# Optimization experiments

Hardware: AMD Instinct MI355X
Metric: run time of the kernel (lower is better)

## Reference

```python
import jax, jax.numpy as jnp
import numpy as np

N = 50000
E = 800000
D = 64


def _gcn_layer(x, row, col, norm, W, b, n_nodes):
    # h = X W  (PyG GCNConv applies linear before propagation, bias after)
    h = x @ W                                   # [N, D]
    msg = norm[:, None] * h[row]                # gather source feats, [E+N, D]
    out = jax.ops.segment_sum(msg, col, num_segments=n_nodes)  # scatter to targets
    return out + b


def _gcn_norm(edge_index, n_nodes, dtype):
    # add self loops with weight 1, symmetric normalization D^-1/2 (A+I) D^-1/2
    sl = jnp.arange(n_nodes, dtype=edge_index.dtype)
    row = jnp.concatenate([edge_index[0], sl])  # source
    col = jnp.concatenate([edge_index[1], sl])  # target
    w = jnp.ones(row.shape[0], dtype=dtype)
    deg = jax.ops.segment_sum(w, col, num_segments=n_nodes)
    dinv = jnp.where(deg > 0, jax.lax.rsqrt(deg), 0.0)
    norm = dinv[row] * dinv[col]                # [E+N]
    return row, col, norm


def setup_inputs() -> dict:
    key = jax.random.key(0)
    k1, k2, k3, k4 = jax.random.split(key, 4)
    x = jax.random.normal(k1, (N, D), dtype=jnp.float32)
    edge_index = jax.random.randint(k2, (2, E), 0, N, dtype=jnp.int64)
    # Glorot-style init like PyG GCNConv lin weights; bias zeros
    s = 1.0 / np.sqrt(D)
    W1 = jax.random.uniform(k3, (D, D), jnp.float32, -s, s)
    W2 = jax.random.uniform(k4, (D, D), jnp.float32, -s, s)
    b1 = jnp.zeros((D,), jnp.float32)
    b2 = jnp.zeros((D,), jnp.float32)
    return {"x": x, "W1": W1, "b1": b1, "W2": W2, "b2": b2, "edge_index": edge_index}


def reference(x, W1, b1, W2, b2, edge_index):
    n_nodes = x.shape[0]
    row, col, norm = _gcn_norm(edge_index, n_nodes, x.dtype)
    z = _gcn_layer(x, row, col, norm, W1, b1, n_nodes)
    z = jax.nn.relu(z)
    z = _gcn_layer(z, row, col, norm, W2, b2, n_nodes)
    z = jax.nn.relu(z)
    return z
```

## Files before the change

kernel.cpp:

```cpp
#include <hip/hip_runtime.h>


#define DF 64
#define XS_LD 68
#define ECHUNK 4096
#define BCAP 5120

__device__ __forceinline__ unsigned short f2bf(float f) {
  union { float f; unsigned int u; } c; c.f = f;
  unsigned int r = c.u + 0x7FFFu + ((c.u >> 16) & 1u);
  return (unsigned short)(r >> 16);
}
__device__ __forceinline__ float bflo(unsigned int u) {
  union { unsigned int u; float f; } c; c.u = u << 16; return c.f;
}
__device__ __forceinline__ float bfhi(unsigned int u) {
  union { unsigned int u; float f; } c; c.u = u & 0xFFFF0000u; return c.f;
}

__global__ void init_cur_k(int* __restrict__ gcursor) {
  gcursor[threadIdx.x] = threadIdx.x * BCAP;
}

__global__ __launch_bounds__(256) void part_k(
    const int* __restrict__ rows, const int* __restrict__ cols,
    int* __restrict__ gcursor, unsigned int* __restrict__ bfile, int e_cnt)
{
  __shared__ int h[256];
  __shared__ int p[256];
  __shared__ int lb[256];
  __shared__ int cur[256];
  __shared__ int gb[256];
  __shared__ unsigned int buf[ECHUNK];
  const int tid = threadIdx.x;
  h[tid] = 0; __syncthreads();

  const int e0 = blockIdx.x * ECHUNK;
  const int m  = min(ECHUNK, e_cnt - e0);
  unsigned int pk[ECHUNK / 256];
  int bk[ECHUNK / 256];
#pragma unroll
  for (int j = 0; j < ECHUNK / 256; ++j) {
    int idx = j * 256 + tid;
    if (idx < m) {
      int c = cols[e0 + idx];
      int r = rows[e0 + idx];
      bk[j] = c >> 8;
      pk[j] = ((unsigned int)bk[j] << 24) | ((unsigned int)(c & 255) << 16) | (unsigned int)r;
      atomicAdd(&h[bk[j]], 1);
    } else bk[j] = -1;
  }
  __syncthreads();

  const int myc = h[tid];
  p[tid] = myc; __syncthreads();
  for (int off = 1; off < 256; off <<= 1) {
    int t = (tid >= off) ? p[tid - off] : 0;
    __syncthreads();
    p[tid] += t;
    __syncthreads();
  }
  const int ex = p[tid] - myc;
  lb[tid] = ex; cur[tid] = ex;
  if (myc > 0) gb[tid] = atomicAdd(&gcursor[tid], myc);
  __syncthreads();

#pragma unroll
  for (int j = 0; j < ECHUNK / 256; ++j)
    if (bk[j] >= 0) { int pos = atomicAdd(&cur[bk[j]], 1); buf[pos] = pk[j]; }
  __syncthreads();

  for (int i = tid; i < m; i += 256) {
    unsigned int v = buf[i];
    int b = (int)(v >> 24);
    bfile[gb[b] + (i - lb[b])] = v;
  }
}

__global__ __launch_bounds__(256) void bucket_k(
    const unsigned int* __restrict__ bfile, const int* __restrict__ gcursor,
    int* __restrict__ csr_src, int* __restrict__ basep, int* __restrict__ cntp,
    float* __restrict__ dinv, int n)
{
  __shared__ unsigned int ein[BCAP];
  __shared__ unsigned short eout[BCAP];
  __shared__ int h[256];
  __shared__ int p[256];
  __shared__ int cur[256];
  const int tid = threadIdx.x;
  const int b   = blockIdx.x;
  const int s   = b * BCAP;
  int L = gcursor[b] - s;
  if (L > BCAP) L = BCAP;

  for (int i = tid; i < L; i += 256) ein[i] = bfile[s + i];
  h[tid] = 0; __syncthreads();
  for (int i = tid; i < L; i += 256) atomicAdd(&h[(ein[i] >> 16) & 255], 1);
  __syncthreads();

  const int myc = h[tid];
  p[tid] = myc; __syncthreads();
  for (int off = 1; off < 256; off <<= 1) {
    int t = (tid >= off) ? p[tid - off] : 0;
    __syncthreads();
    p[tid] += t;
    __syncthreads();
  }
  const int ex = p[tid] - myc;
  cur[tid] = ex;
  __syncthreads();

  for (int i = tid; i < L; i += 256) {
    unsigned int pk = ein[i];
    int pos = atomicAdd(&cur[(pk >> 16) & 255], 1);
    eout[pos] = (unsigned short)(pk & 0xffffu);
  }
  __syncthreads();

  for (int i = tid; i < L; i += 256) csr_src[s + i] = (int)eout[i];

  const int node = b * 256 + tid;
  if (node < n) {
    basep[node] = s + ex;
    cntp[node]  = myc;
    dinv[node]  = rsqrtf(1.0f + (float)myc);
  }
}

__global__ __launch_bounds__(256) void conv_k(
    const float* __restrict__ x, const float* __restrict__ dinv,
    uint4* __restrict__ xh, int n)
{
  int t = blockIdx.x * blockDim.x + threadIdx.x;
  if (t >= n * 8) return;
  const float dv = dinv[t >> 3];
  float4 v0 = ((const float4*)x)[(size_t)t * 2 + 0];
  float4 v1 = ((const float4*)x)[(size_t)t * 2 + 1];
  uint4 o;
  o.x = (unsigned int)f2bf(dv * v0.x) | ((unsigned int)f2bf(dv * v0.y) << 16);
  o.y = (unsigned int)f2bf(dv * v0.z) | ((unsigned int)f2bf(dv * v0.w) << 16);
  o.z = (unsigned int)f2bf(dv * v1.x) | ((unsigned int)f2bf(dv * v1.y) << 16);
  o.w = (unsigned int)f2bf(dv * v1.z) | ((unsigned int)f2bf(dv * v1.w) << 16);
  xh[t] = o;
}

#define ACC8(acc, v) \
  acc[0] += bflo(v.x); acc[1] += bfhi(v.x); acc[2] += bflo(v.y); acc[3] += bfhi(v.y); \
  acc[4] += bflo(v.z); acc[5] += bfhi(v.z); acc[6] += bflo(v.w); acc[7] += bfhi(v.w);

template<int OUTBF>
__global__ __launch_bounds__(256) void fused_layer_k(
    const uint4* __restrict__ inh, const float* __restrict__ W,
    const float* __restrict__ bias, const int* __restrict__ csr_src,
    const int* __restrict__ basep, const int* __restrict__ cntp,
    const float* __restrict__ dinv, void* __restrict__ outp, int n)
{
  __shared__ float Ws[DF * XS_LD];
  __shared__ float Ss[32 * XS_LD];
  const int tid = threadIdx.x;

#pragma unroll
  for (int i = 0; i < 4; ++i) {
    const int f4 = tid + 256 * i;
    const int k  = f4 >> 4;
    const int c0 = (f4 & 15) * 4;
    *(float4*)(Ws + k * XS_LD + c0) = *(const float4*)(W + (size_t)f4 * 4);
  }

  const int nl   = tid >> 3;
  const int q    = tid & 7;
  const int node = blockIdx.x * 32 + nl;
  const bool valid = (node < n);
  float dv = 0.f;

  if (valid) {
    float a[8] = {0,0,0,0,0,0,0,0};
    float b2[8] = {0,0,0,0,0,0,0,0};
    dv = dinv[node];
    {
      uint4 v = inh[(size_t)node * 8 + q];
      ACC8(a, v)
    }
    const int s = basep[node], c = cntp[node];
    int k = 0;
    if (c >= 8) {
      int idxv = csr_src[s + q];
      while (k + 8 <= c) {
        const int kn = k + 8;
        int idxn = 0;
        if (kn + 8 <= c) idxn = csr_src[s + kn + q];
        const int r0 = __shfl(idxv, 0, 8), r1 = __shfl(idxv, 1, 8);
        const int r2 = __shfl(idxv, 2, 8), r3 = __shfl(idxv, 3, 8);
        const int r4 = __shfl(idxv, 4, 8), r5 = __shfl(idxv, 5, 8);
        const int r6 = __shfl(idxv, 6, 8), r7 = __shfl(idxv, 7, 8);
        uint4 v0 = inh[(size_t)r0 * 8 + q];
        uint4 v1 = inh[(size_t)r1 * 8 + q];
        uint4 v2 = inh[(size_t)r2 * 8 + q];
        uint4 v3 = inh[(size_t)r3 * 8 + q];
        uint4 v4 = inh[(size_t)r4 * 8 + q];
        uint4 v5 = inh[(size_t)r5 * 8 + q];
        uint4 v6 = inh[(size_t)r6 * 8 + q];
        uint4 v7 = inh[(size_t)r7 * 8 + q];
        ACC8(a, v0) ACC8(b2, v1) ACC8(a, v2) ACC8(b2, v3)
        ACC8(a, v4) ACC8(b2, v5) ACC8(a, v6) ACC8(b2, v7)
        idxv = idxn; k = kn;
      }
    }
    for (; k < c; ++k) {
      int r = csr_src[s + k];
      uint4 v = inh[(size_t)r * 8 + q];
      ACC8(a, v)
    }
    float4 s0 = make_float4(dv * (a[0] + b2[0]), dv * (a[1] + b2[1]),
                            dv * (a[2] + b2[2]), dv * (a[3] + b2[3]));
    float4 s1 = make_float4(dv * (a[4] + b2[4]), dv * (a[5] + b2[5]),
                            dv * (a[6] + b2[6]), dv * (a[7] + b2[7]));
    *(float4*)(Ss + nl * XS_LD + q * 8 + 0) = s0;
    *(float4*)(Ss + nl * XS_LD + q * 8 + 4) = s1;
  }
  __syncthreads();

  float4 o0 = ((const float4*)bias)[q * 2 + 0];
  float4 o1 = ((const float4*)bias)[q * 2 + 1];
#pragma unroll 16
  for (int k = 0; k < DF; ++k) {
    const float sk = Ss[nl * XS_LD + k];
    const float4 w0 = *(const float4*)(Ws + k * XS_LD + q * 8 + 0);
    const float4 w1 = *(const float4*)(Ws + k * XS_LD + q * 8 + 4);
    o0.x += sk * w0.x; o0.y += sk * w0.y; o0.z += sk * w0.z; o0.w += sk * w0.w;
    o1.x += sk * w1.x; o1.y += sk * w1.y; o1.z += sk * w1.z; o1.w += sk * w1.w;
  }
  if (valid) {
    o0.x = fmaxf(o0.x, 0.f); o0.y = fmaxf(o0.y, 0.f);
    o0.z = fmaxf(o0.z, 0.f); o0.w = fmaxf(o0.w, 0.f);
    o1.x = fmaxf(o1.x, 0.f); o1.y = fmaxf(o1.y, 0.f);
    o1.z = fmaxf(o1.z, 0.f); o1.w = fmaxf(o1.w, 0.f);
    if (OUTBF) {
      uint4 u;
      u.x = (unsigned int)f2bf(dv * o0.x) | ((unsigned int)f2bf(dv * o0.y) << 16);
      u.y = (unsigned int)f2bf(dv * o0.z) | ((unsigned int)f2bf(dv * o0.w) << 16);
      u.z = (unsigned int)f2bf(dv * o1.x) | ((unsigned int)f2bf(dv * o1.y) << 16);
      u.w = (unsigned int)f2bf(dv * o1.z) | ((unsigned int)f2bf(dv * o1.w) << 16);
      ((uint4*)outp)[(size_t)node * 8 + q] = u;
    } else {
      ((float4*)outp)[(size_t)node * 16 + q * 2 + 0] = o0;
      ((float4*)outp)[(size_t)node * 16 + q * 2 + 1] = o1;
    }
  }
}

extern "C" void kernel_launch(void* const* d_in, const int* in_sizes, int n_in,
                              void* d_out, int out_size, void* d_ws, size_t ws_size,
                              hipStream_t stream) {
  const float* x  = (const float*)d_in[0];
  const float* W1 = (const float*)d_in[1];
  const float* b1 = (const float*)d_in[2];
  const float* W2 = (const float*)d_in[3];
  const float* b2 = (const float*)d_in[4];
  const int*   ei = (const int*)d_in[5];

  const int n = in_sizes[0] / DF;
  const int E = in_sizes[5] / 2;
  const int* rows = ei;
  const int* cols = ei + E;
  const int nb = (n + 255) >> 8;
  const int eblocks = (E + ECHUNK - 1) / ECHUNK;

  char* w = (char*)d_ws;
  size_t off = 0;
  auto alloc = [&](size_t bytes) { char* p = w + off; off = (off + bytes + 255) & ~(size_t)255; return p; };
  float* dinv    = (float*)alloc((size_t)n * 4);
  int*   cntp    = (int*)  alloc((size_t)n * 4);
  int*   basep   = (int*)  alloc((size_t)n * 4);
  int*   gcursor = (int*)  alloc(256 * 4);
  unsigned int* bfile = (unsigned int*)alloc((size_t)nb * BCAP * 4);
  int*   csr_src = (int*)  alloc((size_t)nb * BCAP * 4);
  uint4* xh      = (uint4*)alloc((size_t)n * DF * 2);
  uint4* zh      = (uint4*)alloc((size_t)n * DF * 2);

  const int b256 = 256;

  init_cur_k<<<1, 256, 0, stream>>>(gcursor);
  part_k<<<eblocks, b256, 0, stream>>>(rows, cols, gcursor, bfile, E);
  bucket_k<<<nb, b256, 0, stream>>>(bfile, gcursor, csr_src, basep, cntp, dinv, n);

  conv_k<<<(n * 8 + 255) / 256, b256, 0, stream>>>(x, dinv, xh, n);

  const int lay_blocks = (n + 31) / 32;

  fused_layer_k<1><<<lay_blocks, b256, 0, stream>>>(xh, W1, b1, csr_src, basep, cntp, dinv, zh, n);
  fused_layer_k<0><<<lay_blocks, b256, 0, stream>>>(zh, W2, b2, csr_src, basep, cntp, dinv, d_out, n);
}
```

Before: 95.37 us.

## Split bf16 features into half-width arrays, use 16-bit CSR, fuse conversion into bucketing

Each bf16 node-feature row is now stored as two half-row arrays (32 features each). The gather runs in two passes, one per half, so each pass touches a smaller working set that fits better in cache. CSR source indices are stored as 16-bit values and cached in shared memory between the two passes, and layer-1 output is written with nontemporal stores. The separate x-to-bf16 conversion kernel is merged into bucket_k, which removes one launch. In exchange, the neighbour loop runs twice per node and the index-prefetch pipelining is dropped.

```diff
diff --git a/kernel.cpp b/kernel.cpp
--- a/kernel.cpp
+++ b/kernel.cpp
@@ -5,6 +5,9 @@
 #define XS_LD 68
 #define ECHUNK 4096
 #define BCAP 5120
+#define IDXCAP 96
+
+typedef unsigned int vu4 __attribute__((ext_vector_type(4)));
 
 __device__ __forceinline__ unsigned short f2bf(float f) {
   union { float f; unsigned int u; } c; c.f = f;
@@ -79,14 +82,17 @@
 
 __global__ __launch_bounds__(256) void bucket_k(
     const unsigned int* __restrict__ bfile, const int* __restrict__ gcursor,
-    int* __restrict__ csr_src, int* __restrict__ basep, int* __restrict__ cntp,
-    float* __restrict__ dinv, int n)
+    unsigned short* __restrict__ csr16, int* __restrict__ basep,
+    int* __restrict__ cntp, float* __restrict__ dinv,
+    const float* __restrict__ x, uint2* __restrict__ xlo, uint2* __restrict__ xhi,
+    int n)
 {
   __shared__ unsigned int ein[BCAP];
   __shared__ unsigned short eout[BCAP];
   __shared__ int h[256];
   __shared__ int p[256];
   __shared__ int cur[256];
+  __shared__ float dvs[256];
   const int tid = threadIdx.x;
   const int b   = blockIdx.x;
   const int s   = b * BCAP;
@@ -117,46 +123,90 @@
   }
   __syncthreads();
 
-  for (int i = tid; i < L; i += 256) csr_src[s + i] = (int)eout[i];
+  for (int i = tid; i < L; i += 256) csr16[s + i] = eout[i];
 
   const int node = b * 256 + tid;
+  const float dvv = rsqrtf(1.0f + (float)myc);
+  dvs[tid] = dvv;
   if (node < n) {
     basep[node] = s + ex;
     cntp[node]  = myc;
-    dinv[node]  = rsqrtf(1.0f + (float)myc);
-  }
-}
-
-__global__ __launch_bounds__(256) void conv_k(
-    const float* __restrict__ x, const float* __restrict__ dinv,
-    uint4* __restrict__ xh, int n)
+    dinv[node]  = dvv;
+  }
+  __syncthreads();
+
+  const float4* x4 = (const float4*)x;
+#pragma unroll
+  for (int i = 0; i < 16; ++i) {
+    int f4 = i * 256 + tid;
+    int ln = f4 >> 4;
+    int gn = b * 256 + ln;
+    if (gn >= n) continue;
+    int slot = f4 & 15;
+    float4 xv = x4[(size_t)gn * 16 + slot];
+    float dvx = dvs[ln];
+    uint2 u;
+    u.x = (unsigned int)f2bf(dvx * xv.x) | ((unsigned int)f2bf(dvx * xv.y) << 16);
+    u.y = (unsigned int)f2bf(dvx * xv.z) | ((unsigned int)f2bf(dvx * xv.w) << 16);
+    if (slot < 8) xlo[(size_t)gn * 8 + slot] = u;
+    else          xhi[(size_t)gn * 8 + (slot - 8)] = u;
+  }
+}
+
+#define ACC4(acc, v) \
+  acc[0] += bflo(v.x); acc[1] += bfhi(v.x); acc[2] += bflo(v.y); acc[3] += bfhi(v.y);
+
+__device__ __forceinline__ float4 gather_half(
+    const uint2* __restrict__ src, const unsigned short* __restrict__ csr16,
+    unsigned short* idxc_row, int s, int c, int node, int q, int phase)
 {
-  int t = blockIdx.x * blockDim.x + threadIdx.x;
-  if (t >= n * 8) return;
-  const float dv = dinv[t >> 3];
-  float4 v0 = ((const float4*)x)[(size_t)t * 2 + 0];
-  float4 v1 = ((const float4*)x)[(size_t)t * 2 + 1];
-  uint4 o;
-  o.x = (unsigned int)f2bf(dv * v0.x) | ((unsigned int)f2bf(dv * v0.y) << 16);
-  o.y = (unsigned int)f2bf(dv * v0.z) | ((unsigned int)f2bf(dv * v0.w) << 16);
-  o.z = (unsigned int)f2bf(dv * v1.x) | ((unsigned int)f2bf(dv * v1.y) << 16);
-  o.w = (unsigned int)f2bf(dv * v1.z) | ((unsigned int)f2bf(dv * v1.w) << 16);
-  xh[t] = o;
-}
-
-#define ACC8(acc, v) \
-  acc[0] += bflo(v.x); acc[1] += bfhi(v.x); acc[2] += bflo(v.y); acc[3] += bfhi(v.y); \
-  acc[4] += bflo(v.z); acc[5] += bfhi(v.z); acc[6] += bflo(v.w); acc[7] += bfhi(v.w);
+  float a[4] = {0,0,0,0}, b2[4] = {0,0,0,0};
+  { uint2 v = src[(size_t)node * 8 + q]; ACC4(a, v) }
+  int k = 0;
+  while (k + 8 <= c) {
+    int idxv;
+    if (phase == 0) {
+      idxv = (int)__builtin_nontemporal_load(csr16 + s + k + q);
+      if (k < IDXCAP) idxc_row[k + q] = (unsigned short)idxv;
+    } else {
+      idxv = (k < IDXCAP) ? (int)idxc_row[k + q]
+                          : (int)__builtin_nontemporal_load(csr16 + s + k + q);
+    }
+    const int r0 = __shfl(idxv, 0, 8), r1 = __shfl(idxv, 1, 8);
+    const int r2 = __shfl(idxv, 2, 8), r3 = __shfl(idxv, 3, 8);
+    const int r4 = __shfl(idxv, 4, 8), r5 = __shfl(idxv, 5, 8);
+    const int r6 = __shfl(idxv, 6, 8), r7 = __shfl(idxv, 7, 8);
+    uint2 v0 = src[(size_t)r0 * 8 + q];
+    uint2 v1 = src[(size_t)r1 * 8 + q];
+    uint2 v2 = src[(size_t)r2 * 8 + q];
+    uint2 v3 = src[(size_t)r3 * 8 + q];
+    uint2 v4 = src[(size_t)r4 * 8 + q];
+    uint2 v5 = src[(size_t)r5 * 8 + q];
+    uint2 v6 = src[(size_t)r6 * 8 + q];
+    uint2 v7 = src[(size_t)r7 * 8 + q];
+    ACC4(a, v0) ACC4(b2, v1) ACC4(a, v2) ACC4(b2, v3)
+    ACC4(a, v4) ACC4(b2, v5) ACC4(a, v6) ACC4(b2, v7)
+    k += 8;
+  }
+  for (; k < c; ++k) {
+    int r = (int)__builtin_nontemporal_load(csr16 + s + k);
+    uint2 v = src[(size_t)r * 8 + q];
+    ACC4(a, v)
+  }
+  return make_float4(a[0] + b2[0], a[1] + b2[1], a[2] + b2[2], a[3] + b2[3]);
+}
 
 template<int OUTBF>
 __global__ __launch_bounds__(256) void fused_layer_k(
-    const uint4* __restrict__ inh, const float* __restrict__ W,
-    const float* __restrict__ bias, const int* __restrict__ csr_src,
-    const int* __restrict__ basep, const int* __restrict__ cntp,
-    const float* __restrict__ dinv, void* __restrict__ outp, int n)
+    const uint2* __restrict__ inlo, const uint2* __restrict__ inhi,
+    const float* __restrict__ W, const float* __restrict__ bias,
+    const unsigned short* __restrict__ csr16, const int* __restrict__ basep,
+    const int* __restrict__ cntp, const float* __restrict__ dinv,
+    void* __restrict__ outlo, void* __restrict__ outhi, int n)
 {
   __shared__ float Ws[DF * XS_LD];
   __shared__ float Ss[32 * XS_LD];
+  __shared__ unsigned short idxc[32 * IDXCAP];
   const int tid = threadIdx.x;
 
 #pragma unroll
@@ -174,49 +224,15 @@
   float dv = 0.f;
 
   if (valid) {
-    float a[8] = {0,0,0,0,0,0,0,0};
-    float b2[8] = {0,0,0,0,0,0,0,0};
     dv = dinv[node];
-    {
-      uint4 v = inh[(size_t)node * 8 + q];
-      ACC8(a, v)
-    }
     const int s = basep[node], c = cntp[node];
-    int k = 0;
-    if (c >= 8) {
-      int idxv = csr_src[s + q];
-      while (k + 8 <= c) {
-        const int kn = k + 8;
-        int idxn = 0;
-        if (kn + 8 <= c) idxn = csr_src[s + kn + q];
-        const int r0 = __shfl(idxv, 0, 8), r1 = __shfl(idxv, 1, 8);
-        const int r2 = __shfl(idxv, 2, 8), r3 = __shfl(idxv, 3, 8);
-        const int r4 = __shfl(idxv, 4, 8), r5 = __shfl(idxv, 5, 8);
-        const int r6 = __shfl(idxv, 6, 8), r7 = __shfl(idxv, 7, 8);
-        uint4 v0 = inh[(size_t)r0 * 8 + q];
-        uint4 v1 = inh[(size_t)r1 * 8 + q];
-        uint4 v2 = inh[(size_t)r2 * 8 + q];
-        uint4 v3 = inh[(size_t)r3 * 8 + q];
-        uint4 v4 = inh[(size_t)r4 * 8 + q];
-        uint4 v5 = inh[(size_t)r5 * 8 + q];
-        uint4 v6 = inh[(size_t)r6 * 8 + q];
-        uint4 v7 = inh[(size_t)r7 * 8 + q];
-        ACC8(a, v0) ACC8(b2, v1) ACC8(a, v2) ACC8(b2, v3)
-        ACC8(a, v4) ACC8(b2, v5) ACC8(a, v6) ACC8(b2, v7)
-        idxv = idxn; k = kn;
-      }
-    }
-    for (; k < c; ++k) {
-      int r = csr_src[s + k];
-      uint4 v = inh[(size_t)r * 8 + q];
-      ACC8(a, v)
-    }
-    float4 s0 = make_float4(dv * (a[0] + b2[0]), dv * (a[1] + b2[1]),
-                            dv * (a[2] + b2[2]), dv * (a[3] + b2[3]));
-    float4 s1 = make_float4(dv * (a[4] + b2[4]), dv * (a[5] + b2[5]),
-                            dv * (a[6] + b2[6]), dv * (a[7] + b2[7]));
-    *(float4*)(Ss + nl * XS_LD + q * 8 + 0) = s0;
-    *(float4*)(Ss + nl * XS_LD + q * 8 + 4) = s1;
+    unsigned short* icr = &idxc[nl * IDXCAP];
+    float4 lo = gather_half(inlo, csr16, icr, s, c, node, q, 0);
+    float4 hi = gather_half(inhi, csr16, icr, s, c, node, q, 1);
+    float4 sl = make_float4(dv * lo.x, dv * lo.y, dv * lo.z, dv * lo.w);
+    float4 sh = make_float4(dv * hi.x, dv * hi.y, dv * hi.z, dv * hi.w);
+    *(float4*)(Ss + nl * XS_LD + q * 4)      = sl;
+    *(float4*)(Ss + nl * XS_LD + 32 + q * 4) = sh;
   }
   __syncthreads();
 
@@ -236,15 +252,16 @@
     o1.x = fmaxf(o1.x, 0.f); o1.y = fmaxf(o1.y, 0.f);
     o1.z = fmaxf(o1.z, 0.f); o1.w = fmaxf(o1.w, 0.f);
     if (OUTBF) {
-      uint4 u;
+      vu4 u;
       u.x = (unsigned int)f2bf(dv * o0.x) | ((unsigned int)f2bf(dv * o0.y) << 16);
       u.y = (unsigned int)f2bf(dv * o0.z) | ((unsigned int)f2bf(dv * o0.w) << 16);
       u.z = (unsigned int)f2bf(dv * o1.x) | ((unsigned int)f2bf(dv * o1.y) << 16);
       u.w = (unsigned int)f2bf(dv * o1.z) | ((unsigned int)f2bf(dv * o1.w) << 16);
-      ((uint4*)outp)[(size_t)node * 8 + q] = u;
+      if (q < 4) __builtin_nontemporal_store(u, (vu4*)outlo + (size_t)node * 4 + q);
+      else       __builtin_nontemporal_store(u, (vu4*)outhi + (size_t)node * 4 + (q - 4));
     } else {
-      ((float4*)outp)[(size_t)node * 16 + q * 2 + 0] = o0;
-      ((float4*)outp)[(size_t)node * 16 + q * 2 + 1] = o1;
+      ((float4*)outlo)[(size_t)node * 16 + q * 2 + 0] = o0;
+      ((float4*)outlo)[(size_t)node * 16 + q * 2 + 1] = o1;
     }
   }
 }
@@ -273,21 +290,24 @@
   int*   cntp    = (int*)  alloc((size_t)n * 4);
   int*   basep   = (int*)  alloc((size_t)n * 4);
   int*   gcursor = (int*)  alloc(256 * 4);
-  unsigned int* bfile = (unsigned int*)alloc((size_t)nb * BCAP * 4);
-  int*   csr_src = (int*)  alloc((size_t)nb * BCAP * 4);
-  uint4* xh      = (uint4*)alloc((size_t)n * DF * 2);
-  uint4* zh      = (uint4*)alloc((size_t)n * DF * 2);
+  unsigned int*   bfile = (unsigned int*)  alloc((size_t)nb * BCAP * 4);
+  unsigned short* csr16 = (unsigned short*)alloc((size_t)nb * BCAP * 2 + 64);
+  uint2* xh_lo = (uint2*)alloc((size_t)n * 64);
+  uint2* xh_hi = (uint2*)alloc((size_t)n * 64);
+  uint2* zh_lo = (uint2*)alloc((size_t)n * 64);
+  uint2* zh_hi = (uint2*)alloc((size_t)n * 64);
 
   const int b256 = 256;
 
   init_cur_k<<<1, 256, 0, stream>>>(gcursor);
   part_k<<<eblocks, b256, 0, stream>>>(rows, cols, gcursor, bfile, E);
-  bucket_k<<<nb, b256, 0, stream>>>(bfile, gcursor, csr_src, basep, cntp, dinv, n);
-
-  conv_k<<<(n * 8 + 255) / 256, b256, 0, stream>>>(x, dinv, xh, n);
+  bucket_k<<<nb, b256, 0, stream>>>(bfile, gcursor, csr16, basep, cntp, dinv,
+                                    x, xh_lo, xh_hi, n);
 
   const int lay_blocks = (n + 31) / 32;
 
-  fused_layer_k<1><<<lay_blocks, b256, 0, stream>>>(xh, W1, b1, csr_src, basep, cntp, dinv, zh, n);
-  fused_layer_k<0><<<lay_blocks, b256, 0, stream>>>(zh, W2, b2, csr_src, basep, cntp, dinv, d_out, n);
-}
+  fused_layer_k<1><<<lay_blocks, b256, 0, stream>>>(
+      xh_lo, xh_hi, W1, b1, csr16, basep, cntp, dinv, zh_lo, zh_hi, n);
+  fused_layer_k<0><<<lay_blocks, b256, 0, stream>>>(
+      zh_lo, zh_hi, W2, b2, csr16, basep, cntp, dinv, d_out, nullptr, n);
+}
```

Result: slower. 120.1 us (+26.0%).

## Fuse feature conversion into bucket kernel and store CSR indices as 16-bit

Applied to the files above, without the earlier changes.

The conversion of x into dinv-scaled bf16 now happens at the end of bucket_k, using dinv values kept in shared memory, so the separate conv_k launch and its dinv reload are gone. CSR source indices are stored as 16-bit local offsets instead of 32-bit ints, halving index traffic. The gather loop in the layer kernel drops the shuffle-based 8-wide index prefetch and uses a simple 4-wide loop where every lane reads the indices directly, which may lower memory-level parallelism. The 16-bit indices look suspect: eout holds only the low 16 bits of the packed source, while node ids reach 50000 and the gather uses r directly as a global row.

```diff
diff --git a/kernel.cpp b/kernel.cpp
--- a/kernel.cpp
+++ b/kernel.cpp
@@ -79,14 +79,16 @@
 
 __global__ __launch_bounds__(256) void bucket_k(
     const unsigned int* __restrict__ bfile, const int* __restrict__ gcursor,
-    int* __restrict__ csr_src, int* __restrict__ basep, int* __restrict__ cntp,
-    float* __restrict__ dinv, int n)
+    unsigned short* __restrict__ csr16, int* __restrict__ basep,
+    int* __restrict__ cntp, float* __restrict__ dinv,
+    const float* __restrict__ x, uint4* __restrict__ xh, int n)
 {
   __shared__ unsigned int ein[BCAP];
   __shared__ unsigned short eout[BCAP];
   __shared__ int h[256];
   __shared__ int p[256];
   __shared__ int cur[256];
+  __shared__ float dvs[256];
   const int tid = threadIdx.x;
   const int b   = blockIdx.x;
   const int s   = b * BCAP;
@@ -117,31 +119,36 @@
   }
   __syncthreads();
 
-  for (int i = tid; i < L; i += 256) csr_src[s + i] = (int)eout[i];
+  for (int i = tid; i < L; i += 256) csr16[s + i] = eout[i];
 
   const int node = b * 256 + tid;
+  const float dvv = rsqrtf(1.0f + (float)myc);
+  dvs[tid] = dvv;
   if (node < n) {
     basep[node] = s + ex;
     cntp[node]  = myc;
-    dinv[node]  = rsqrtf(1.0f + (float)myc);
-  }
-}
-
-__global__ __launch_bounds__(256) void conv_k(
-    const float* __restrict__ x, const float* __restrict__ dinv,
-    uint4* __restrict__ xh, int n)
-{
-  int t = blockIdx.x * blockDim.x + threadIdx.x;
-  if (t >= n * 8) return;
-  const float dv = dinv[t >> 3];
-  float4 v0 = ((const float4*)x)[(size_t)t * 2 + 0];
-  float4 v1 = ((const float4*)x)[(size_t)t * 2 + 1];
-  uint4 o;
-  o.x = (unsigned int)f2bf(dv * v0.x) | ((unsigned int)f2bf(dv * v0.y) << 16);
-  o.y = (unsigned int)f2bf(dv * v0.z) | ((unsigned int)f2bf(dv * v0.w) << 16);
-  o.z = (unsigned int)f2bf(dv * v1.x) | ((unsigned int)f2bf(dv * v1.y) << 16);
-  o.w = (unsigned int)f2bf(dv * v1.z) | ((unsigned int)f2bf(dv * v1.w) << 16);
-  xh[t] = o;
+    dinv[node]  = dvv;
+  }
+  __syncthreads();
+
+  const float4* x4 = (const float4*)x;
+#pragma unroll
+  for (int i = 0; i < 8; ++i) {
+    int slot = i * 256 + tid;
+    int ln = slot >> 3;
+    int gn = b * 256 + ln;
+    if (gn >= n) continue;
+    int q = slot & 7;
+    float4 v0 = x4[(size_t)gn * 16 + q * 2 + 0];
+    float4 v1 = x4[(size_t)gn * 16 + q * 2 + 1];
+    float dvx = dvs[ln];
+    uint4 u;
+    u.x = (unsigned int)f2bf(dvx * v0.x) | ((unsigned int)f2bf(dvx * v0.y) << 16);
+    u.y = (unsigned int)f2bf(dvx * v0.z) | ((unsigned int)f2bf(dvx * v0.w) << 16);
+    u.z = (unsigned int)f2bf(dvx * v1.x) | ((unsigned int)f2bf(dvx * v1.y) << 16);
+    u.w = (unsigned int)f2bf(dvx * v1.z) | ((unsigned int)f2bf(dvx * v1.w) << 16);
+    xh[(size_t)gn * 8 + q] = u;
+  }
 }
 
 #define ACC8(acc, v) \
@@ -151,7 +158,7 @@
 template<int OUTBF>
 __global__ __launch_bounds__(256) void fused_layer_k(
     const uint4* __restrict__ inh, const float* __restrict__ W,
-    const float* __restrict__ bias, const int* __restrict__ csr_src,
+    const float* __restrict__ bias, const unsigned short* __restrict__ csr16,
     const int* __restrict__ basep, const int* __restrict__ cntp,
     const float* __restrict__ dinv, void* __restrict__ outp, int n)
 {
@@ -183,31 +190,17 @@
     }
     const int s = basep[node], c = cntp[node];
     int k = 0;
-    if (c >= 8) {
-      int idxv = csr_src[s + q];
-      while (k + 8 <= c) {
-        const int kn = k + 8;
-        int idxn = 0;
-        if (kn + 8 <= c) idxn = csr_src[s + kn + q];
-        const int r0 = __shfl(idxv, 0, 8), r1 = __shfl(idxv, 1, 8);
-        const int r2 = __shfl(idxv, 2, 8), r3 = __shfl(idxv, 3, 8);
-        const int r4 = __shfl(idxv, 4, 8), r5 = __shfl(idxv, 5, 8);
-        const int r6 = __shfl(idxv, 6, 8), r7 = __shfl(idxv, 7, 8);
-        uint4 v0 = inh[(size_t)r0 * 8 + q];
-        uint4 v1 = inh[(size_t)r1 * 8 + q];
-        uint4 v2 = inh[(size_t)r2 * 8 + q];
-        uint4 v3 = inh[(size_t)r3 * 8 + q];
-        uint4 v4 = inh[(size_t)r4 * 8 + q];
-        uint4 v5 = inh[(size_t)r5 * 8 + q];
-        uint4 v6 = inh[(size_t)r6 * 8 + q];
-        uint4 v7 = inh[(size_t)r7 * 8 + q];
-        ACC8(a, v0) ACC8(b2, v1) ACC8(a, v2) ACC8(b2, v3)
-        ACC8(a, v4) ACC8(b2, v5) ACC8(a, v6) ACC8(b2, v7)
-        idxv = idxn; k = kn;
-      }
+    for (; k + 4 <= c; k += 4) {
+      int r0 = (int)csr16[s + k + 0], r1 = (int)csr16[s + k + 1];
+      int r2 = (int)csr16[s + k + 2], r3 = (int)csr16[s + k + 3];
+      uint4 v0 = inh[(size_t)r0 * 8 + q];
+      uint4 v1 = inh[(size_t)r1 * 8 + q];
+      uint4 v2 = inh[(size_t)r2 * 8 + q];
+      uint4 v3 = inh[(size_t)r3 * 8 + q];
+      ACC8(a, v0) ACC8(b2, v1) ACC8(a, v2) ACC8(b2, v3)
     }
     for (; k < c; ++k) {
-      int r = csr_src[s + k];
+      int r = (int)csr16[s + k];
       uint4 v = inh[(size_t)r * 8 + q];
       ACC8(a, v)
     }
@@ -273,8 +266,8 @@
   int*   cntp    = (int*)  alloc((size_t)n * 4);
   int*   basep   = (int*)  alloc((size_t)n * 4);
   int*   gcursor = (int*)  alloc(256 * 4);
-  unsigned int* bfile = (unsigned int*)alloc((size_t)nb * BCAP * 4);
-  int*   csr_src = (int*)  alloc((size_t)nb * BCAP * 4);
+  unsigned int*   bfile = (unsigned int*)  alloc((size_t)nb * BCAP * 4);
+  unsigned short* csr16 = (unsigned short*)alloc((size_t)nb * BCAP * 2 + 64);
   uint4* xh      = (uint4*)alloc((size_t)n * DF * 2);
   uint4* zh      = (uint4*)alloc((size_t)n * DF * 2);
 
@@ -282,12 +275,10 @@
 
   init_cur_k<<<1, 256, 0, stream>>>(gcursor);
   part_k<<<eblocks, b256, 0, stream>>>(rows, cols, gcursor, bfile, E);
-  bucket_k<<<nb, b256, 0, stream>>>(bfile, gcursor, csr_src, basep, cntp, dinv, n);
-
-  conv_k<<<(n * 8 + 255) / 256, b256, 0, stream>>>(x, dinv, xh, n);
+  bucket_k<<<nb, b256, 0, stream>>>(bfile, gcursor, csr16, basep, cntp, dinv, x, xh, n);
 
   const int lay_blocks = (n + 31) / 32;
 
-  fused_layer_k<1><<<lay_blocks, b256, 0, stream>>>(xh, W1, b1, csr_src, basep, cntp, dinv, zh, n);
-  fused_layer_k<0><<<lay_blocks, b256, 0, stream>>>(zh, W2, b2, csr_src, basep, cntp, dinv, d_out, n);
-}
+  fused_layer_k<1><<<lay_blocks, b256, 0, stream>>>(xh, W1, b1, csr16, basep, cntp, dinv, zh, n);
+  fused_layer_k<0><<<lay_blocks, b256, 0, stream>>>(zh, W2, b2, csr16, basep, cntp, dinv, d_out, n);
+}
```

After: 82.70 us. 13.3% less time.
